# Optimization experiments

Measured on AMD Instinct MI355X. Metric: run time of the kernel, lower is better.

The kernel has to match this reference:

```python
import jax, jax.numpy as jnp
import numpy as np

D = 256
N = 4096


def setup_inputs() -> dict:
    key = jax.random.key(0)
    k0, k1, k2, k3, k4 = jax.random.split(key, 5)
    x0 = jax.random.normal(k0, (N, D), dtype=jnp.float32)
    x1 = jax.random.normal(k1, (N, D), dtype=jnp.float32)
    C_norm = jax.random.normal(k2, (D, D), dtype=jnp.float32)
    # Stacked params of the d Linear(1, d) layers: W[i, j] = weight of layer i
    # mapping scalar input to output unit j; B[i, j] = its bias.
    W = jax.random.normal(k3, (D, D), dtype=jnp.float32) * 0.1
    B = jax.random.normal(k4, (D, D), dtype=jnp.float32) * 0.1
    return {"x0": x0, "x1": x1, "C_norm": C_norm, "W": W, "B": B}


def reference(x0, x1, C_norm, W, B):
    # Original: y[i, j, k] = W[i, j] * x0[k, i] + B[i, j] + C_norm[i, j]
    # then cat x1^T (as a (1, d, n) slab) in front and take max over axis 0.
    # y: (d, d, n)
    y = W[:, :, None] * x0.T[:, None, :] + (B + C_norm)[:, :, None]
    m = jnp.max(y, axis=0)              # (d, n): max over the d source layers
    out = jnp.maximum(m, x1.T)          # include the x1 slab in the max
    return out.T                        # (n, d)
```

## Files before the change

### kernel.cpp

```cpp
#include <hip/hip_runtime.h>


typedef _Float16 h16;
typedef h16 h2  __attribute__((ext_vector_type(2)));
typedef h16 h8v __attribute__((ext_vector_type(8)));
typedef float f32x4 __attribute__((ext_vector_type(4)));

constexpr int Dk = 256;

struct __align__(16) Chunk {
  h16 W[64 * 64];
  h16 A[64 * 64];
  h16 X0[64 * 64];
};

__global__ __launch_bounds__(512, 2)
void mp_kernel(const float* __restrict__ x0, const float* __restrict__ x1,
               const float* __restrict__ Cn, const float* __restrict__ Wg,
               const float* __restrict__ Bg, float* __restrict__ out) {
  __shared__ Chunk buf[2];

  const int tid = threadIdx.x;
  const int w   = tid >> 6;
  const int l   = tid & 63;
  const int tk  = l >> 3;
  const int tj  = l & 7;
  const int kb  = blockIdx.x >> 2;
  const int jb  = blockIdx.x & 3;
  const int k0  = kb * 64;
  const int j0  = jb * 64;

  const int srow = tid >> 3;
  const int scol = (tid & 7) * 8;
  const int xsw  = scol ^ ((srow >> 3) << 3);

  h2 acc[8][4];
#pragma unroll
  for (int kk = 0; kk < 8; ++kk)
#pragma unroll
    for (int jp = 0; jp < 4; ++jp)
      acc[kk][jp] = h2{(h16)(-60000.0f), (h16)(-60000.0f)};

  auto stage = [&](int c, Chunk* b) {
    const int i0 = 64 * c;
    const f32x4* wg = reinterpret_cast<const f32x4*>(&Wg[(i0 + srow) * Dk + j0 + scol]);
    const f32x4* bg = reinterpret_cast<const f32x4*>(&Bg[(i0 + srow) * Dk + j0 + scol]);
    const f32x4* cg = reinterpret_cast<const f32x4*>(&Cn[(i0 + srow) * Dk + j0 + scol]);
    const f32x4* xg = reinterpret_cast<const f32x4*>(&x0[(k0 + srow) * Dk + i0 + scol]);
    const f32x4 wv0 = wg[0], wv1 = wg[1];
    const f32x4 av0 = bg[0] + cg[0], av1 = bg[1] + cg[1];
    const f32x4 xv0 = xg[0], xv1 = xg[1];
    h8v hw, ha, hx;
#pragma unroll
    for (int u = 0; u < 4; ++u) {
      hw[u] = (h16)wv0[u];  hw[u + 4] = (h16)wv1[u];
      ha[u] = (h16)av0[u];  ha[u + 4] = (h16)av1[u];
      hx[u] = (h16)xv0[u];  hx[u + 4] = (h16)xv1[u];
    }
    *reinterpret_cast<h8v*>(&b->W [srow * 64 + scol]) = hw;
    *reinterpret_cast<h8v*>(&b->A [srow * 64 + scol]) = ha;
    *reinterpret_cast<h8v*>(&b->X0[srow * 64 + xsw])  = hx;
  };

  auto compute = [&](Chunk* b) {
    const int iloc = 8 * w;
    h8v xr[8];
#pragma unroll
    for (int kk = 0; kk < 8; ++kk)
      xr[kk] = *reinterpret_cast<const h8v*>(
          &b->X0[(tk * 8 + kk) * 64 + (iloc ^ (tk << 3))]);
#pragma unroll
    for (int ii = 0; ii < 8; ++ii) {
      const h8v wv = *reinterpret_cast<const h8v*>(&b->W[(iloc + ii) * 64 + tj * 8]);
      const h8v av = *reinterpret_cast<const h8v*>(&b->A[(iloc + ii) * 64 + tj * 8]);
      const h2 wp0 = __builtin_shufflevector(wv, wv, 0, 1);
      const h2 wp1 = __builtin_shufflevector(wv, wv, 2, 3);
      const h2 wp2 = __builtin_shufflevector(wv, wv, 4, 5);
      const h2 wp3 = __builtin_shufflevector(wv, wv, 6, 7);
      const h2 ap0 = __builtin_shufflevector(av, av, 0, 1);
      const h2 ap1 = __builtin_shufflevector(av, av, 2, 3);
      const h2 ap2 = __builtin_shufflevector(av, av, 4, 5);
      const h2 ap3 = __builtin_shufflevector(av, av, 6, 7);
#pragma unroll
      for (int kk = 0; kk < 8; ++kk) {
        const h16 e = xr[kk][ii];
        const h2 xb = h2{e, e};
        acc[kk][0] = __builtin_elementwise_max(acc[kk][0], __builtin_elementwise_fma(wp0, xb, ap0));
        acc[kk][1] = __builtin_elementwise_max(acc[kk][1], __builtin_elementwise_fma(wp1, xb, ap1));
        acc[kk][2] = __builtin_elementwise_max(acc[kk][2], __builtin_elementwise_fma(wp2, xb, ap2));
        acc[kk][3] = __builtin_elementwise_max(acc[kk][3], __builtin_elementwise_fma(wp3, xb, ap3));
      }
    }
  };

  stage(0, &buf[0]);
  __syncthreads();
#pragma unroll
  for (int c = 0; c < 4; ++c) {
    if (c < 3) stage(c + 1, &buf[(c + 1) & 1]);
    compute(&buf[c & 1]);
    __syncthreads();
  }

  uint4* mrg = reinterpret_cast<uint4*>(&buf[0]);

  auto wslot = [&](int s) {
#pragma unroll
    for (int kk = 0; kk < 8; ++kk) {
      uint4 u;
      u.x = __builtin_bit_cast(unsigned int, acc[kk][0]);
      u.y = __builtin_bit_cast(unsigned int, acc[kk][1]);
      u.z = __builtin_bit_cast(unsigned int, acc[kk][2]);
      u.w = __builtin_bit_cast(unsigned int, acc[kk][3]);
      mrg[(s * 8 + kk) * 64 + l] = u;
    }
  };
  auto rmerge = [&](int s) {
#pragma unroll
    for (int kk = 0; kk < 8; ++kk) {
      const uint4 u = mrg[(s * 8 + kk) * 64 + l];
      acc[kk][0] = __builtin_elementwise_max(acc[kk][0], __builtin_bit_cast(h2, u.x));
      acc[kk][1] = __builtin_elementwise_max(acc[kk][1], __builtin_bit_cast(h2, u.y));
      acc[kk][2] = __builtin_elementwise_max(acc[kk][2], __builtin_bit_cast(h2, u.z));
      acc[kk][3] = __builtin_elementwise_max(acc[kk][3], __builtin_bit_cast(h2, u.w));
    }
  };

  if (w >= 4) wslot(w - 4);
  __syncthreads();
  if (w < 4) rmerge(w);
  __syncthreads();
  if (w == 2 || w == 3) wslot(w - 2);
  __syncthreads();
  if (w < 2) rmerge(w);
  __syncthreads();
  if (w == 1) wslot(0);
  __syncthreads();
  if (w == 0) { rmerge(0); wslot(0); }
  __syncthreads();

  {
    const uint4 u = mrg[w * 64 + l];
    const h2 p0 = __builtin_bit_cast(h2, u.x);
    const h2 p1 = __builtin_bit_cast(h2, u.y);
    const h2 p2 = __builtin_bit_cast(h2, u.z);
    const h2 p3 = __builtin_bit_cast(h2, u.w);
    const int k = k0 + (l >> 3) * 8 + w;
    const int j = j0 + (l & 7) * 8;
    f32x4 o0 = { (float)p0[0], (float)p0[1], (float)p1[0], (float)p1[1] };
    f32x4 o1 = { (float)p2[0], (float)p2[1], (float)p3[0], (float)p3[1] };
    const f32x4* xg = reinterpret_cast<const f32x4*>(&x1[k * Dk + j]);
    o0 = __builtin_elementwise_max(o0, xg[0]);
    o1 = __builtin_elementwise_max(o1, xg[1]);
    f32x4* og = reinterpret_cast<f32x4*>(&out[k * Dk + j]);
    og[0] = o0;
    og[1] = o1;
  }
}

extern "C" void kernel_launch(void* const* d_in, const int* in_sizes, int n_in,
                              void* d_out, int out_size, void* d_ws, size_t ws_size,
                              hipStream_t stream) {
  const float* x0 = (const float*)d_in[0];
  const float* x1 = (const float*)d_in[1];
  const float* Cn = (const float*)d_in[2];
  const float* W  = (const float*)d_in[3];
  const float* Bm = (const float*)d_in[4];
  float* out = (float*)d_out;

  const int n = in_sizes[0] / Dk;
  const int grid = (n / 64) * 4;
  hipLaunchKernelGGL(mp_kernel, dim3(grid), dim3(512), 0, stream,
                     x0, x1, Cn, W, Bm, out);
}
```

Measured before the change: 19.24 us.

## Split fp16 conversion into prep kernel and load full tiles into LDS once

Adds a prep kernel that converts x0 to fp16 and W and B+C to fp16 into workspace. The main kernel then loads the full 256-row W/A slices and the 64x256 x0 slab into shared memory in one pass, and each warp processes 32 i values instead of using a double-buffered 4-chunk pipeline. The aim is to halve global read bytes and drop the per-block conversion and per-chunk syncs. In exchange it adds a second launch, a workspace round trip, and 96KB of LDS, which limits occupancy to one block per CU.

```diff
diff --git a/kernel.cpp b/kernel.cpp
--- a/kernel.cpp
+++ b/kernel.cpp
@@ -8,102 +8,122 @@
 
 constexpr int Dk = 256;
 
-struct __align__(16) Chunk {
-  h16 W[64 * 64];
-  h16 A[64 * 64];
-  h16 X0[64 * 64];
-};
-
-__global__ __launch_bounds__(512, 2)
-void mp_kernel(const float* __restrict__ x0, const float* __restrict__ x1,
-               const float* __restrict__ Cn, const float* __restrict__ Wg,
-               const float* __restrict__ Bg, float* __restrict__ out) {
-  __shared__ Chunk buf[2];
+__global__ __launch_bounds__(256)
+void prep(const float* __restrict__ x0, const float* __restrict__ Cn,
+          const float* __restrict__ W, const float* __restrict__ Bm,
+          h16* __restrict__ x0h, h16* __restrict__ Wh, h16* __restrict__ Ah) {
+  const int b = blockIdx.x;
+  const int t = threadIdx.x;
+  if (b < 512) {
+    const int idx = (b * 256 + t) * 8;
+    const f32x4 v0 = *reinterpret_cast<const f32x4*>(&x0[idx]);
+    const f32x4 v1 = *reinterpret_cast<const f32x4*>(&x0[idx + 4]);
+    h8v h;
+#pragma unroll
+    for (int u = 0; u < 4; ++u) { h[u] = (h16)v0[u]; h[u + 4] = (h16)v1[u]; }
+    *reinterpret_cast<h8v*>(&x0h[idx]) = h;
+  } else {
+    const int idx = ((b - 512) * 256 + t) * 8;
+    const f32x4 w0 = *reinterpret_cast<const f32x4*>(&W[idx]);
+    const f32x4 w1 = *reinterpret_cast<const f32x4*>(&W[idx + 4]);
+    const f32x4 b0 = *reinterpret_cast<const f32x4*>(&Bm[idx]);
+    const f32x4 b1 = *reinterpret_cast<const f32x4*>(&Bm[idx + 4]);
+    const f32x4 c0 = *reinterpret_cast<const f32x4*>(&Cn[idx]);
+    const f32x4 c1 = *reinterpret_cast<const f32x4*>(&Cn[idx + 4]);
+    const f32x4 a0 = b0 + c0, a1 = b1 + c1;
+    h8v hw, ha;
+#pragma unroll
+    for (int u = 0; u < 4; ++u) {
+      hw[u] = (h16)w0[u]; hw[u + 4] = (h16)w1[u];
+      ha[u] = (h16)a0[u]; ha[u + 4] = (h16)a1[u];
+    }
+    *reinterpret_cast<h8v*>(&Wh[idx]) = hw;
+    *reinterpret_cast<h8v*>(&Ah[idx]) = ha;
+  }
+}
+
+__global__ __launch_bounds__(512, 1)
+void mp_main(const h16* __restrict__ x0h, const h16* __restrict__ Wh,
+             const h16* __restrict__ Ah, const float* __restrict__ x1,
+             float* __restrict__ out) {
+  __shared__ h16 Wl[256 * 64];
+  __shared__ h16 Al[256 * 64];
+  __shared__ h16 Xl[64 * 256];
 
   const int tid = threadIdx.x;
   const int w   = tid >> 6;
   const int l   = tid & 63;
   const int tk  = l >> 3;
   const int tj  = l & 7;
-  const int kb  = blockIdx.x >> 2;
-  const int jb  = blockIdx.x & 3;
-  const int k0  = kb * 64;
-  const int j0  = jb * 64;
-
-  const int srow = tid >> 3;
-  const int scol = (tid & 7) * 8;
-  const int xsw  = scol ^ ((srow >> 3) << 3);
+  const int k0  = (blockIdx.x >> 2) * 64;
+  const int j0  = (blockIdx.x & 3) * 64;
+
+#pragma unroll
+  for (int c = 0; c < 4; ++c) {
+    const int idx = c * 512 + tid;
+    const int row = idx >> 3;
+    const int col = (idx & 7) * 8;
+    *reinterpret_cast<h8v*>(&Wl[row * 64 + col]) =
+        *reinterpret_cast<const h8v*>(&Wh[row * Dk + j0 + col]);
+    *reinterpret_cast<h8v*>(&Al[row * 64 + col]) =
+        *reinterpret_cast<const h8v*>(&Ah[row * Dk + j0 + col]);
+  }
+#pragma unroll
+  for (int c = 0; c < 4; ++c) {
+    const int idx = c * 512 + tid;
+    const int row = idx >> 5;
+    const int col = (idx & 31) * 8;
+    const int sw  = col ^ (((row >> 3) & 7) * 8);
+    *reinterpret_cast<h8v*>(&Xl[row * 256 + sw]) =
+        *reinterpret_cast<const h8v*>(&x0h[(k0 + row) * Dk + col]);
+  }
+  __syncthreads();
 
   h2 acc[8][4];
 #pragma unroll
   for (int kk = 0; kk < 8; ++kk)
 #pragma unroll
-    for (int jp = 0; jp < 4; ++jp)
-      acc[kk][jp] = h2{(h16)(-60000.0f), (h16)(-60000.0f)};
-
-  auto stage = [&](int c, Chunk* b) {
-    const int i0 = 64 * c;
-    const f32x4* wg = reinterpret_cast<const f32x4*>(&Wg[(i0 + srow) * Dk + j0 + scol]);
-    const f32x4* bg = reinterpret_cast<const f32x4*>(&Bg[(i0 + srow) * Dk + j0 + scol]);
-    const f32x4* cg = reinterpret_cast<const f32x4*>(&Cn[(i0 + srow) * Dk + j0 + scol]);
-    const f32x4* xg = reinterpret_cast<const f32x4*>(&x0[(k0 + srow) * Dk + i0 + scol]);
-    const f32x4 wv0 = wg[0], wv1 = wg[1];
-    const f32x4 av0 = bg[0] + cg[0], av1 = bg[1] + cg[1];
-    const f32x4 xv0 = xg[0], xv1 = xg[1];
-    h8v hw, ha, hx;
-#pragma unroll
-    for (int u = 0; u < 4; ++u) {
-      hw[u] = (h16)wv0[u];  hw[u + 4] = (h16)wv1[u];
-      ha[u] = (h16)av0[u];  ha[u + 4] = (h16)av1[u];
-      hx[u] = (h16)xv0[u];  hx[u + 4] = (h16)xv1[u];
-    }
-    *reinterpret_cast<h8v*>(&b->W [srow * 64 + scol]) = hw;
-    *reinterpret_cast<h8v*>(&b->A [srow * 64 + scol]) = ha;
-    *reinterpret_cast<h8v*>(&b->X0[srow * 64 + xsw])  = hx;
-  };
-
-  auto compute = [&](Chunk* b) {
-    const int iloc = 8 * w;
+    for (int p = 0; p < 4; ++p)
+      acc[kk][p] = h2{(h16)(-60000.0f), (h16)(-60000.0f)};
+
+  const int ibase = 32 * w;
+
+#define USTEP(U) {                                                              \
+    const h8v wv = *reinterpret_cast<const h8v*>(&Wl[(ic + (U)) * 64 + tj * 8]);\
+    const h8v av = *reinterpret_cast<const h8v*>(&Al[(ic + (U)) * 64 + tj * 8]);\
+    const h2 wp0 = __builtin_shufflevector(wv, wv, 0, 1);                       \
+    const h2 wp1 = __builtin_shufflevector(wv, wv, 2, 3);                       \
+    const h2 wp2 = __builtin_shufflevector(wv, wv, 4, 5);                       \
+    const h2 wp3 = __builtin_shufflevector(wv, wv, 6, 7);                       \
+    const h2 ap0 = __builtin_shufflevector(av, av, 0, 1);                       \
+    const h2 ap1 = __builtin_shufflevector(av, av, 2, 3);                       \
+    const h2 ap2 = __builtin_shufflevector(av, av, 4, 5);                       \
+    const h2 ap3 = __builtin_shufflevector(av, av, 6, 7);                       \
+    _Pragma("unroll")                                                           \
+    for (int kk = 0; kk < 8; ++kk) {                                            \
+      const h2 xb = __builtin_shufflevector(xr[kk], xr[kk], (U), (U));          \
+      acc[kk][0] = __builtin_elementwise_max(acc[kk][0], __builtin_elementwise_fma(wp0, xb, ap0)); \
+      acc[kk][1] = __builtin_elementwise_max(acc[kk][1], __builtin_elementwise_fma(wp1, xb, ap1)); \
+      acc[kk][2] = __builtin_elementwise_max(acc[kk][2], __builtin_elementwise_fma(wp2, xb, ap2)); \
+      acc[kk][3] = __builtin_elementwise_max(acc[kk][3], __builtin_elementwise_fma(wp3, xb, ap3)); \
+    }                                                                           \
+  }
+
+#pragma unroll
+  for (int g = 0; g < 4; ++g) {
+    const int ic = ibase + g * 8;
     h8v xr[8];
 #pragma unroll
-    for (int kk = 0; kk < 8; ++kk)
-      xr[kk] = *reinterpret_cast<const h8v*>(
-          &b->X0[(tk * 8 + kk) * 64 + (iloc ^ (tk << 3))]);
-#pragma unroll
-    for (int ii = 0; ii < 8; ++ii) {
-      const h8v wv = *reinterpret_cast<const h8v*>(&b->W[(iloc + ii) * 64 + tj * 8]);
-      const h8v av = *reinterpret_cast<const h8v*>(&b->A[(iloc + ii) * 64 + tj * 8]);
-      const h2 wp0 = __builtin_shufflevector(wv, wv, 0, 1);
-      const h2 wp1 = __builtin_shufflevector(wv, wv, 2, 3);
-      const h2 wp2 = __builtin_shufflevector(wv, wv, 4, 5);
-      const h2 wp3 = __builtin_shufflevector(wv, wv, 6, 7);
-      const h2 ap0 = __builtin_shufflevector(av, av, 0, 1);
-      const h2 ap1 = __builtin_shufflevector(av, av, 2, 3);
-      const h2 ap2 = __builtin_shufflevector(av, av, 4, 5);
-      const h2 ap3 = __builtin_shufflevector(av, av, 6, 7);
-#pragma unroll
-      for (int kk = 0; kk < 8; ++kk) {
-        const h16 e = xr[kk][ii];
-        const h2 xb = h2{e, e};
-        acc[kk][0] = __builtin_elementwise_max(acc[kk][0], __builtin_elementwise_fma(wp0, xb, ap0));
-        acc[kk][1] = __builtin_elementwise_max(acc[kk][1], __builtin_elementwise_fma(wp1, xb, ap1));
-        acc[kk][2] = __builtin_elementwise_max(acc[kk][2], __builtin_elementwise_fma(wp2, xb, ap2));
-        acc[kk][3] = __builtin_elementwise_max(acc[kk][3], __builtin_elementwise_fma(wp3, xb, ap3));
-      }
-    }
-  };
-
-  stage(0, &buf[0]);
-  __syncthreads();
-#pragma unroll
-  for (int c = 0; c < 4; ++c) {
-    if (c < 3) stage(c + 1, &buf[(c + 1) & 1]);
-    compute(&buf[c & 1]);
-    __syncthreads();
-  }
-
-  uint4* mrg = reinterpret_cast<uint4*>(&buf[0]);
-
+    for (int kk = 0; kk < 8; ++kk) {
+      const int row = tk * 8 + kk;
+      xr[kk] = *reinterpret_cast<const h8v*>(&Xl[row * 256 + (ic ^ (tk * 8))]);
+    }
+    USTEP(0) USTEP(1) USTEP(2) USTEP(3) USTEP(4) USTEP(5) USTEP(6) USTEP(7)
+  }
+#undef USTEP
+  __syncthreads();
+
+  uint4* mrg = reinterpret_cast<uint4*>(Wl);
   auto wslot = [&](int s) {
 #pragma unroll
     for (int kk = 0; kk < 8; ++kk) {
@@ -169,7 +189,12 @@
   float* out = (float*)d_out;
 
   const int n = in_sizes[0] / Dk;
-  const int grid = (n / 64) * 4;
-  hipLaunchKernelGGL(mp_kernel, dim3(grid), dim3(512), 0, stream,
-                     x0, x1, Cn, W, Bm, out);
+  h16* x0h = (h16*)d_ws;
+  h16* Wh  = (h16*)((char*)d_ws + (size_t)n * Dk * 2);
+  h16* Ah  = (h16*)((char*)d_ws + (size_t)n * Dk * 2 + Dk * Dk * 2);
+
+  hipLaunchKernelGGL(prep, dim3(512 + 32), dim3(256), 0, stream,
+                     x0, Cn, W, Bm, x0h, Wh, Ah);
+  hipLaunchKernelGGL(mp_main, dim3((n / 64) * 4), dim3(512), 0, stream,
+                     x0h, Wh, Ah, x1, out);
 }
```

After: 23.96 us. +24.6%, slower.
